# Optimization experiments

Measured on AMD Instinct MI355X. Metric: run time of the kernel, lower is better.

## Reference

```python
import jax, jax.numpy as jnp
from jax import lax
import numpy as np

DN = ('NCHW', 'OIHW', 'NCHW')


def _conv(x, w, b):
    y = lax.conv_general_dilated(x, w, (1, 1), 'SAME', dimension_numbers=DN)
    return y + b[None, :, None, None]


def setup_inputs() -> dict:
    key = jax.random.key(0)
    ks = jax.random.split(key, 8)
    B = 2
    noise = 0.1 * jax.random.normal(ks[0], (B, 768, 577), dtype=jnp.float32)  # N(0, 0.1)
    targets = jax.random.randint(ks[1], (B, 384, 384), 0, 171)
    w1 = 0.02 * jax.random.normal(ks[2], (512, 768, 3, 3), dtype=jnp.float32)
    b1 = 0.02 * jax.random.normal(ks[3], (512,), dtype=jnp.float32)
    w2 = 0.02 * jax.random.normal(ks[4], (512, 512, 3, 3), dtype=jnp.float32)
    b2 = 0.02 * jax.random.normal(ks[5], (512,), dtype=jnp.float32)
    w3 = 0.2 * jax.random.normal(ks[6], (77,), dtype=jnp.float32)  # Con3: Conv2d(1,77,1x1)
    b3 = 0.2 * jax.random.normal(ks[7], (77,), dtype=jnp.float32)
    return {'noise': noise, 'targets': targets, 'w1': w1, 'b1': b1,
            'w2': w2, 'b2': b2, 'w3': w3, 'b3': b3}


def reference(noise, targets, w1, b1, w2, b2, w3, b3):
    B = noise.shape[0]
    # NoiseToImage is shadowed by an empty nn.Sequential() -> identity
    image_noise = jnp.transpose(noise, (2, 0, 1))  # (577, B, 768)

    # --- NoiseToText ---
    H, W = targets.shape[1], targets.shape[2]
    ih = (jnp.arange(24) * H) // 24  # nearest-neighbor interpolate indices
    iw = (jnp.arange(24) * W) // 24
    m = targets[:, ih][:, :, iw]  # (B, 24, 24) class labels
    # one-hot scatter into 256 channels, keep first 171 (labels >=171 -> all-zero)
    mask = (m[:, None] == jnp.arange(171)[None, :, None, None]).astype(noise.dtype)  # (B,171,24,24)

    x = noise[:, :, 1:].reshape(B, 768, 24, 24)  # drop CLS token
    xm = x[:, None] * mask[:, :, None]            # (B,171,768,24,24)
    xm = xm.reshape(B * 171, 768, 24, 24)

    y = _conv(xm, w1, b1)                         # (B*171,512,24,24)
    y = y.reshape(-1, 512, 6, 4, 6, 4).mean(axis=(3, 5))  # AdaptiveAvgPool2d((6,6))
    y = _conv(y, w2, b2)                          # (B*171,512,6,6)
    y = y.mean(axis=(2, 3))                       # AdaptiveAvgPool2d((1,1)) -> (B*171,512)
    y = y.reshape(B, 171, 1, 512).transpose(0, 2, 1, 3)  # (B,1,171,512)
    # Con3: 1x1 conv with in_channels=1, out_channels=77
    text_noise = w3[None, :, None, None] * y + b3[None, :, None, None]  # (B,77,171,512)
    return image_noise, text_noise
```

## Files before the change

### kernel.cpp

```cpp
#include <hip/hip_runtime.h>
#include <hip/hip_bf16.h>

typedef unsigned short u16;
typedef short bf16x8 __attribute__((ext_vector_type(8)));
typedef float f32x4 __attribute__((ext_vector_type(4)));

__device__ __forceinline__ u16 f2bf(float f){
    unsigned u = __float_as_uint(f);
    unsigned r = 0x7fffu + ((u >> 16) & 1u);
    return (u16)((u + r) >> 16);
}

__device__ __forceinline__ void gload_lds16(const u16* g, u16* lds_base){
    __builtin_amdgcn_global_load_lds(
        (const __attribute__((address_space(1))) unsigned int*)g,
        (__attribute__((address_space(3))) unsigned int*)lds_base, 16, 0, 0);
}

__device__ __forceinline__ void wgbar(){
    asm volatile("" ::: "memory");
    __builtin_amdgcn_s_barrier();
    asm volatile("" ::: "memory");
}

#define OUT0_N 886272
#define OUT1_N 13483008
#define YN 175104
#define KS2 12

__global__ void k_prep(const float* __restrict__ noise, const int* __restrict__ targets,
                       const float* __restrict__ w1, const float* __restrict__ b1,
                       const float* __restrict__ w2,
                       float* __restrict__ out0, u16* __restrict__ XbfT,
                       u16* __restrict__ Are, u16* __restrict__ Mfull16,
                       float* __restrict__ biasH, int* __restrict__ labels,
                       u16* __restrict__ Zcat16){
    __shared__ float sh[32 * 33];
    int blk = blockIdx.x;
    int tid = threadIdx.x;
    if (blk < 912){
        int b   = blk / 456;
        int rem = blk % 456;
        int cb  = rem / 19, sb = rem % 19;
        int tx = tid & 31, ty = tid >> 5;
        int s0 = sb * 32, c0 = cb * 32;
        float (*tile)[33] = (float(*)[33])sh;
        #pragma unroll
        for (int i = 0; i < 4; i++){
            int c = c0 + ty + i * 8;
            int s = s0 + tx;
            if (s < 577) tile[ty + i * 8][tx] = noise[(size_t)(b * 768 + c) * 577 + s];
        }
        __syncthreads();
        #pragma unroll
        for (int i = 0; i < 4; i++){
            int s = s0 + ty + i * 8;
            int c = c0 + tx;
            if (s >= 577) continue;
            float v = tile[tx][ty + i * 8];
            out0[(size_t)(s * 2 + b) * 768 + c] = v;
            if (s >= 1) XbfT[(size_t)(b * 576 + s - 1) * 768 + c] = f2bf(v);
        }
    } else if (blk < 2448){
        int idx = (blk - 912) * 256 + tid;
        int k = idx % 768; int c1 = idx / 768;
        const float* wp = w1 + (size_t)idx * 9;
        #pragma unroll
        for (int tap = 0; tap < 9; tap++)
            Are[(size_t)(c1 * 9 + tap) * 768 + k] = f2bf(wp[tap]);
    } else if (blk < 3472){
        int b2i = blk - 2448;
        int c2 = b2i >> 1, h = b2i & 1;
        int c1 = h * 256 + tid;
        const float* wp = w2 + (size_t)(c2 * 512 + c1) * 9;
        float t[3][3];
        #pragma unroll
        for (int r = 0; r < 3; r++)
            #pragma unroll
            for (int s = 0; s < 3; s++)
                t[r][s] = wp[r * 3 + s];
        float cs0[3], cs1[3], cs2[3];
        #pragma unroll
        for (int r = 0; r < 3; r++){
            cs0[r] = t[r][0] + t[r][1];
            cs1[r] = t[r][0] + t[r][1] + t[r][2];
            cs2[r] = t[r][1] + t[r][2];
        }
        const float inv = 1.0f / 576.0f;
        u16* Mp = Mfull16 + (size_t)(c2 * 512 + c1) * 9;
        Mp[0] = f2bf(inv * (cs0[0] + cs0[1]));
        Mp[1] = f2bf(inv * (cs1[0] + cs1[1]));
        Mp[2] = f2bf(inv * (cs2[0] + cs2[1]));
        Mp[3] = f2bf(inv * (cs0[0] + cs0[1] + cs0[2]));
        Mp[4] = f2bf(inv * (cs1[0] + cs1[1] + cs1[2]));
        Mp[5] = f2bf(inv * (cs2[0] + cs2[1] + cs2[2]));
        Mp[6] = f2bf(inv * (cs0[1] + cs0[2]));
        Mp[7] = f2bf(inv * (cs1[1] + cs1[2]));
        Mp[8] = f2bf(inv * (cs2[1] + cs2[2]));
        float s_cw = 25.f * (t[0][0] + t[0][2] + t[2][0] + t[2][2])
                   + 30.f * (t[0][1] + t[1][0] + t[1][2] + t[2][1])
                   + 36.f * t[1][1];
        sh[tid] = b1[c1] * s_cw;
        __syncthreads();
        for (int o = 128; o > 0; o >>= 1){ if (tid < o) sh[tid] += sh[tid + o]; __syncthreads(); }
        if (tid == 0) biasH[h * 512 + c2] = sh[0] * (1.0f / 36.0f);
    } else if (blk < 3477){
        int idx = (blk - 3472) * 256 + tid;
        if (idx < 1152){
            int b = idx / 576; int p = idx % 576;
            int i = p / 24, j = p % 24;
            labels[idx] = targets[b * 147456 + i * 16 * 384 + j * 16];
        }
    } else {
        int idx = (blk - 3477) * 256 + tid;
        if (idx < 193536) Zcat16[342 * 4608 + idx] = 0;
    }
}

__launch_bounds__(256)
__global__ void k_gemm1(const u16* __restrict__ Are, const u16* __restrict__ XbfT,
                        float* __restrict__ D){
    __shared__ u16 As[2][192 * 64];
    __shared__ u16 Bs[2][128 * 64];
    int tid  = threadIdx.x;
    int wave = tid >> 6, lane = tid & 63;
    int l16 = lane & 15, quad = lane >> 4;
    int wm = wave >> 1, wn = wave & 1;
    int m0 = blockIdx.x * 192;
    int n0 = blockIdx.y * 128;
    int srow = lane >> 3;
    int scol = ((lane & 7) * 8) ^ (srow * 8);
    int rx   = (l16 & 7) * 8;
    const u16* Ag = Are  + (size_t)(m0 + srow) * 768 + scol;
    const u16* Bg = XbfT + (size_t)(n0 + srow) * 768 + scol;
    f32x4 acc[6][4] = {};

    auto stage = [&](int buf, int k0){
        #pragma unroll
        for (int j = 0; j < 6; j++){
            int ch = wave * 6 + j;
            gload_lds16(Ag + (size_t)ch * 8 * 768 + k0, &As[buf][ch * 512]);
        }
        #pragma unroll
        for (int j = 0; j < 4; j++){
            int ch = wave * 4 + j;
            gload_lds16(Bg + (size_t)ch * 8 * 768 + k0, &Bs[buf][ch * 512]);
        }
    };
    auto compute = [&](int buf){
        #pragma unroll
        for (int ks = 0; ks < 2; ks++){
            int kc = (ks * 32 + quad * 8) ^ rx;
            bf16x8 af[6], bf[4];
            #pragma unroll
            for (int i = 0; i < 6; i++)
                af[i] = *(const bf16x8*)&As[buf][(wm * 96 + i * 16 + l16) * 64 + kc];
            #pragma unroll
            for (int i = 0; i < 4; i++)
                bf[i] = *(const bf16x8*)&Bs[buf][(wn * 64 + i * 16 + l16) * 64 + kc];
            #pragma unroll
            for (int mi = 0; mi < 6; mi++)
                #pragma unroll
                for (int ni = 0; ni < 4; ni++)
                    acc[mi][ni] = __builtin_amdgcn_mfma_f32_16x16x32_bf16(af[mi], bf[ni], acc[mi][ni], 0, 0, 0);
        }
    };

    stage(0, 0);
    #pragma unroll 1
    for (int t = 0; t < 10; t += 2){
        stage(1, (t + 1) * 64);
        asm volatile("s_waitcnt vmcnt(10)" ::: "memory");
        wgbar();
        compute(0);
        wgbar();
        stage(0, (t + 2) * 64);
        asm volatile("s_waitcnt vmcnt(10)" ::: "memory");
        wgbar();
        compute(1);
        wgbar();
    }
    stage(1, 11 * 64);
    asm volatile("s_waitcnt vmcnt(10)" ::: "memory");
    wgbar();
    compute(0);
    wgbar();
    asm volatile("s_waitcnt vmcnt(0)" ::: "memory");
    wgbar();
    compute(1);

    #pragma unroll
    for (int mi = 0; mi < 6; mi++)
        #pragma unroll
        for (int ni = 0; ni < 4; ni++)
            #pragma unroll
            for (int r = 0; r < 4; r++)
                D[(size_t)(m0 + wm * 96 + mi * 16 + quad * 4 + r) * 1152 + n0 + wn * 64 + ni * 16 + l16] = acc[mi][ni][r];
}

__launch_bounds__(256)
__global__ void k_scatter(const float* __restrict__ D, const int* __restrict__ labels,
                          u16* __restrict__ Zcat16){
    int blk = blockIdx.x;
    int b  = blk >> 9;
    int c1 = blk & 511;
    __shared__ float acc[171 * 9];
    int t = threadIdx.x;
    for (int q = t; q < 1539; q += 256) acc[q] = 0.f;
    __syncthreads();
    for (int p = t; p < 576; p += 256){
        int cls = labels[b * 576 + p];
        if (cls < 0 || cls >= 171) continue;
        int i = p / 24, j = p % 24;
        float slot[9];
        #pragma unroll
        for (int q = 0; q < 9; q++) slot[q] = 0.f;
        unsigned used = 0;
        int tau[3]; bool vs[3];
        #pragma unroll
        for (int s1 = 0; s1 < 3; s1++){
            int v = j - s1 + 1;
            vs[s1]  = (v >= 0 && v < 24);
            tau[s1] = (v < 4) ? 0 : ((v < 20) ? 1 : 2);
        }
        #pragma unroll
        for (int r1 = 0; r1 < 3; r1++){
            int u = i - r1 + 1;
            if (u < 0 || u >= 24) continue;
            int rho = (u < 4) ? 0 : ((u < 20) ? 1 : 2);
            #pragma unroll
            for (int s1 = 0; s1 < 3; s1++){
                if (!vs[s1]) continue;
                float tv = D[(size_t)(c1 * 9 + r1 * 3 + s1) * 1152 + b * 576 + p];
                int sl = rho * 3 + tau[s1];
                slot[sl] += tv;
                used |= 1u << sl;
            }
        }
        #pragma unroll
        for (int sl = 0; sl < 9; sl++)
            if (used & (1u << sl)) atomicAdd(&acc[cls * 9 + sl], slot[sl]);
    }
    __syncthreads();
    for (int q = t; q < 1539; q += 256){
        int cls = q / 9, sl = q % 9;
        Zcat16[(size_t)(b * 171 + cls) * 4608 + c1 * 9 + sl] = f2bf(acc[q]);
    }
}

__launch_bounds__(256)
__global__ void k_gemm2m(const u16* __restrict__ Zcat16, const u16* __restrict__ Mfull16,
                         float* __restrict__ ypart){
    __shared__ u16 As[128 * 64];
    __shared__ u16 Bs[64 * 64];
    int tid  = threadIdx.x;
    int wave = tid >> 6, lane = tid & 63;
    int l16 = lane & 15, quad = lane >> 4;
    int wm = wave >> 1, wn = wave & 1;
    int m0 = blockIdx.x * 128;
    int n0 = blockIdx.y * 64;
    int kbeg = blockIdx.z * 384;
    int srow = lane >> 3, scol = (lane & 7) * 8;
    f32x4 acc[4][2] = {};
    for (int k0 = kbeg; k0 < kbeg + 384; k0 += 64){
        #pragma unroll
        for (int j = 0; j < 4; j++){
            int ch = wave * 4 + j;
            gload_lds16(Zcat16 + (size_t)(m0 + ch * 8 + srow) * 4608 + k0 + scol, &As[ch * 512]);
        }
        #pragma unroll
        for (int j = 0; j < 2; j++){
            int ch = wave * 2 + j;
            gload_lds16(Mfull16 + (size_t)(n0 + ch * 8 + srow) * 4608 + k0 + scol, &Bs[ch * 512]);
        }
        __syncthreads();
        #pragma unroll
        for (int ks = 0; ks < 2; ks++){
            bf16x8 af[4], bf[2];
            #pragma unroll
            for (int i = 0; i < 4; i++)
                af[i] = *(const bf16x8*)&As[(wm * 64 + i * 16 + l16) * 64 + ks * 32 + quad * 8];
            #pragma unroll
            for (int i = 0; i < 2; i++)
                bf[i] = *(const bf16x8*)&Bs[(wn * 32 + i * 16 + l16) * 64 + ks * 32 + quad * 8];
            #pragma unroll
            for (int mi = 0; mi < 4; mi++)
                #pragma unroll
                for (int ni = 0; ni < 2; ni++)
                    acc[mi][ni] = __builtin_amdgcn_mfma_f32_16x16x32_bf16(af[mi], bf[ni], acc[mi][ni], 0, 0, 0);
        }
        __syncthreads();
    }
    float* yp = ypart + (size_t)blockIdx.z * YN;
    #pragma unroll
    for (int mi = 0; mi < 4; mi++)
        #pragma unroll
        for (int r = 0; r < 4; r++){
            int n = m0 + wm * 64 + mi * 16 + quad * 4 + r;
            if (n >= 342) continue;
            #pragma unroll
            for (int ni = 0; ni < 2; ni++)
                yp[(size_t)n * 512 + n0 + wn * 32 + ni * 16 + l16] = acc[mi][ni][r];
        }
}

__global__ void k_red(const float* __restrict__ ypart, const float* __restrict__ biasH,
                      const float* __restrict__ b2, float4* __restrict__ ysum){
    int idx = blockIdx.x * 128 + threadIdx.x;
    int c4 = idx & 127;
    int n  = idx >> 7;
    float4 sum = ((const float4*)b2)[c4];
    float4 ba  = ((const float4*)biasH)[c4];
    float4 bb  = ((const float4*)biasH)[128 + c4];
    sum.x += ba.x + bb.x; sum.y += ba.y + bb.y; sum.z += ba.z + bb.z; sum.w += ba.w + bb.w;
    #pragma unroll
    for (int s = 0; s < KS2; s++){
        float4 v = *(const float4*)&ypart[(size_t)s * YN + (size_t)n * 512 + c4 * 4];
        sum.x += v.x; sum.y += v.y; sum.z += v.z; sum.w += v.w;
    }
    ysum[idx] = sum;
}

__global__ void k_expand(const float4* __restrict__ ysum, const float* __restrict__ w3,
                         const float* __restrict__ b3, float4* __restrict__ out1){
    int idx = blockIdx.x * 256 + threadIdx.x;
    if (idx >= OUT1_N / 4) return;
    int c4 = idx & 127;
    int t  = idx >> 7;
    int cls = t % 171;
    int u   = t / 171;
    int o   = u % 77;
    int b   = u / 77;
    float w  = w3[o];
    float bb = b3[o];
    float4 v = ysum[(b * 171 + cls) * 128 + c4];
    out1[idx] = make_float4(w * v.x + bb, w * v.y + bb, w * v.z + bb, w * v.w + bb);
}

extern "C" void kernel_launch(void* const* d_in, const int* in_sizes, int n_in,
                              void* d_out, int out_size, void* d_ws, size_t ws_size,
                              hipStream_t stream) {
    const float* noise   = (const float*)d_in[0];
    const int*   targets = (const int*)  d_in[1];
    const float* w1      = (const float*)d_in[2];
    const float* b1      = (const float*)d_in[3];
    const float* w2      = (const float*)d_in[4];
    const float* b2      = (const float*)d_in[5];
    const float* w3      = (const float*)d_in[6];
    const float* b3      = (const float*)d_in[7];
    float* out0 = (float*)d_out;
    float* out1 = out0 + OUT0_N;

    char* ws = (char*)d_ws;
    const size_t OFF_ARE  = 0;
    const size_t OFF_X    = 7077888;
    const size_t OFF_D    = OFF_X   + 1769472;
    const size_t OFF_MF   = OFF_D   + 21233664;
    const size_t OFF_ZC   = OFF_MF  + 4718592;
    const size_t OFF_BH   = OFF_ZC  + 3538944;
    const size_t OFF_LAB  = OFF_BH  + 4096;
    const size_t OFF_YS   = OFF_LAB + 4608;

    u16*   Are    = (u16*)  (ws + OFF_ARE);
    u16*   XbfT   = (u16*)  (ws + OFF_X);
    float* D      = (float*)(ws + OFF_D);
    float* ypart  = (float*)(ws + OFF_D);
    u16*   Mfull16= (u16*)  (ws + OFF_MF);
    u16*   Zcat16 = (u16*)  (ws + OFF_ZC);
    float* biasH  = (float*)(ws + OFF_BH);
    int*   labels = (int*)  (ws + OFF_LAB);
    float* ysum   = (float*)(ws + OFF_YS);

    k_prep  <<<4233, 256, 0, stream>>>(noise, targets, w1, b1, w2,
                                       out0, XbfT, Are, Mfull16, biasH, labels, Zcat16);
    k_gemm1 <<<dim3(24, 9), 256, 0, stream>>>(Are, XbfT, D);
    k_scatter<<<1024, 256, 0, stream>>>(D, labels, Zcat16);
    k_gemm2m<<<dim3(3, 8, KS2), 256, 0, stream>>>(Zcat16, Mfull16, ypart);
    k_red   <<<342, 128, 0, stream>>>(ypart, biasH, b2, (float4*)ysum);
    k_expand<<<13167, 256, 0, stream>>>((const float4*)ysum, w3, b3, (float4*)out1);
}
```

Baseline: 156.2 us.

## Store GEMM1 output as bf16, atomically reduce split-K GEMM2, drop reduction kernel

GEMM1 now writes its intermediate as bf16 instead of fp32, which halves the traffic for that write and for the scatter kernel's reads. GEMM2's split-K partials are atomically added into a zero-initialised ysum (zeroed by extra k_prep blocks), and the bias additions move into k_expand. This removes the separate k_red kernel and its partial buffer. s_setprio is also placed around the MFMA loops. Rounding D to bf16 adds precision loss, and fp32 atomics make the summation order nondeterministic.

```diff
diff --git a/kernel.cpp b/kernel.cpp
--- a/kernel.cpp
+++ b/kernel.cpp
@@ -9,6 +9,9 @@
     unsigned u = __float_as_uint(f);
     unsigned r = 0x7fffu + ((u >> 16) & 1u);
     return (u16)((u + r) >> 16);
+}
+__device__ __forceinline__ float bf2f(u16 h){
+    return __uint_as_float(((unsigned)h) << 16);
 }
 
 __device__ __forceinline__ void gload_lds16(const u16* g, u16* lds_base){
@@ -34,7 +37,7 @@
                        float* __restrict__ out0, u16* __restrict__ XbfT,
                        u16* __restrict__ Are, u16* __restrict__ Mfull16,
                        float* __restrict__ biasH, int* __restrict__ labels,
-                       u16* __restrict__ Zcat16){
+                       u16* __restrict__ Zcat16, float4* __restrict__ ysum){
     __shared__ float sh[32 * 33];
     int blk = blockIdx.x;
     int tid = threadIdx.x;
@@ -111,15 +114,18 @@
             int i = p / 24, j = p % 24;
             labels[idx] = targets[b * 147456 + i * 16 * 384 + j * 16];
         }
-    } else {
+    } else if (blk < 4233){
         int idx = (blk - 3477) * 256 + tid;
         if (idx < 193536) Zcat16[342 * 4608 + idx] = 0;
+    } else {
+        int idx = (blk - 4233) * 256 + tid;
+        ysum[idx] = make_float4(0.f, 0.f, 0.f, 0.f);
     }
 }
 
 __launch_bounds__(256)
 __global__ void k_gemm1(const u16* __restrict__ Are, const u16* __restrict__ XbfT,
-                        float* __restrict__ D){
+                        u16* __restrict__ D){
     __shared__ u16 As[2][192 * 64];
     __shared__ u16 Bs[2][128 * 64];
     int tid  = threadIdx.x;
@@ -158,11 +164,13 @@
             #pragma unroll
             for (int i = 0; i < 4; i++)
                 bf[i] = *(const bf16x8*)&Bs[buf][(wn * 64 + i * 16 + l16) * 64 + kc];
+            __builtin_amdgcn_s_setprio(1);
             #pragma unroll
             for (int mi = 0; mi < 6; mi++)
                 #pragma unroll
                 for (int ni = 0; ni < 4; ni++)
                     acc[mi][ni] = __builtin_amdgcn_mfma_f32_16x16x32_bf16(af[mi], bf[ni], acc[mi][ni], 0, 0, 0);
+            __builtin_amdgcn_s_setprio(0);
         }
     };
 
@@ -195,11 +203,11 @@
         for (int ni = 0; ni < 4; ni++)
             #pragma unroll
             for (int r = 0; r < 4; r++)
-                D[(size_t)(m0 + wm * 96 + mi * 16 + quad * 4 + r) * 1152 + n0 + wn * 64 + ni * 16 + l16] = acc[mi][ni][r];
+                D[(size_t)(m0 + wm * 96 + mi * 16 + quad * 4 + r) * 1152 + n0 + wn * 64 + ni * 16 + l16] = f2bf(acc[mi][ni][r]);
 }
 
 __launch_bounds__(256)
-__global__ void k_scatter(const float* __restrict__ D, const int* __restrict__ labels,
+__global__ void k_scatter(const u16* __restrict__ D, const int* __restrict__ labels,
                           u16* __restrict__ Zcat16){
     int blk = blockIdx.x;
     int b  = blk >> 9;
@@ -231,7 +239,7 @@
             #pragma unroll
             for (int s1 = 0; s1 < 3; s1++){
                 if (!vs[s1]) continue;
-                float tv = D[(size_t)(c1 * 9 + r1 * 3 + s1) * 1152 + b * 576 + p];
+                float tv = bf2f(D[(size_t)(c1 * 9 + r1 * 3 + s1) * 1152 + b * 576 + p]);
                 int sl = rho * 3 + tau[s1];
                 slot[sl] += tv;
                 used |= 1u << sl;
@@ -250,7 +258,7 @@
 
 __launch_bounds__(256)
 __global__ void k_gemm2m(const u16* __restrict__ Zcat16, const u16* __restrict__ Mfull16,
-                         float* __restrict__ ypart){
+                         float* __restrict__ ysum){
     __shared__ u16 As[128 * 64];
     __shared__ u16 Bs[64 * 64];
     int tid  = threadIdx.x;
@@ -283,15 +291,16 @@
             #pragma unroll
             for (int i = 0; i < 2; i++)
                 bf[i] = *(const bf16x8*)&Bs[(wn * 32 + i * 16 + l16) * 64 + ks * 32 + quad * 8];
+            __builtin_amdgcn_s_setprio(1);
             #pragma unroll
             for (int mi = 0; mi < 4; mi++)
                 #pragma unroll
                 for (int ni = 0; ni < 2; ni++)
                     acc[mi][ni] = __builtin_amdgcn_mfma_f32_16x16x32_bf16(af[mi], bf[ni], acc[mi][ni], 0, 0, 0);
+            __builtin_amdgcn_s_setprio(0);
         }
         __syncthreads();
     }
-    float* yp = ypart + (size_t)blockIdx.z * YN;
     #pragma unroll
     for (int mi = 0; mi < 4; mi++)
         #pragma unroll
@@ -300,28 +309,12 @@
             if (n >= 342) continue;
             #pragma unroll
             for (int ni = 0; ni < 2; ni++)
-                yp[(size_t)n * 512 + n0 + wn * 32 + ni * 16 + l16] = acc[mi][ni][r];
-        }
-}
-
-__global__ void k_red(const float* __restrict__ ypart, const float* __restrict__ biasH,
-                      const float* __restrict__ b2, float4* __restrict__ ysum){
-    int idx = blockIdx.x * 128 + threadIdx.x;
-    int c4 = idx & 127;
-    int n  = idx >> 7;
-    float4 sum = ((const float4*)b2)[c4];
-    float4 ba  = ((const float4*)biasH)[c4];
-    float4 bb  = ((const float4*)biasH)[128 + c4];
-    sum.x += ba.x + bb.x; sum.y += ba.y + bb.y; sum.z += ba.z + bb.z; sum.w += ba.w + bb.w;
-    #pragma unroll
-    for (int s = 0; s < KS2; s++){
-        float4 v = *(const float4*)&ypart[(size_t)s * YN + (size_t)n * 512 + c4 * 4];
-        sum.x += v.x; sum.y += v.y; sum.z += v.z; sum.w += v.w;
-    }
-    ysum[idx] = sum;
-}
-
-__global__ void k_expand(const float4* __restrict__ ysum, const float* __restrict__ w3,
+                atomicAdd(&ysum[(size_t)n * 512 + n0 + wn * 32 + ni * 16 + l16], acc[mi][ni][r]);
+        }
+}
+
+__global__ void k_expand(const float4* __restrict__ ysum, const float* __restrict__ biasH,
+                         const float* __restrict__ b2, const float* __restrict__ w3,
                          const float* __restrict__ b3, float4* __restrict__ out1){
     int idx = blockIdx.x * 256 + threadIdx.x;
     if (idx >= OUT1_N / 4) return;
@@ -333,7 +326,14 @@
     int b   = u / 77;
     float w  = w3[o];
     float bb = b3[o];
-    float4 v = ysum[(b * 171 + cls) * 128 + c4];
+    float4 v  = ysum[(b * 171 + cls) * 128 + c4];
+    float4 s2 = ((const float4*)b2)[c4];
+    float4 ba = ((const float4*)biasH)[c4];
+    float4 bc = ((const float4*)biasH)[128 + c4];
+    v.x += s2.x + ba.x + bc.x;
+    v.y += s2.y + ba.y + bc.y;
+    v.z += s2.z + ba.z + bc.z;
+    v.w += s2.w + ba.w + bc.w;
     out1[idx] = make_float4(w * v.x + bb, w * v.y + bb, w * v.z + bb, w * v.w + bb);
 }
 
@@ -355,7 +355,7 @@
     const size_t OFF_ARE  = 0;
     const size_t OFF_X    = 7077888;
     const size_t OFF_D    = OFF_X   + 1769472;
-    const size_t OFF_MF   = OFF_D   + 21233664;
+    const size_t OFF_MF   = OFF_D   + 10616832;
     const size_t OFF_ZC   = OFF_MF  + 4718592;
     const size_t OFF_BH   = OFF_ZC  + 3538944;
     const size_t OFF_LAB  = OFF_BH  + 4096;
@@ -363,19 +363,18 @@
 
     u16*   Are    = (u16*)  (ws + OFF_ARE);
     u16*   XbfT   = (u16*)  (ws + OFF_X);
-    float* D      = (float*)(ws + OFF_D);
-    float* ypart  = (float*)(ws + OFF_D);
+    u16*   D      = (u16*)  (ws + OFF_D);
     u16*   Mfull16= (u16*)  (ws + OFF_MF);
     u16*   Zcat16 = (u16*)  (ws + OFF_ZC);
     float* biasH  = (float*)(ws + OFF_BH);
     int*   labels = (int*)  (ws + OFF_LAB);
     float* ysum   = (float*)(ws + OFF_YS);
 
-    k_prep  <<<4233, 256, 0, stream>>>(noise, targets, w1, b1, w2,
-                                       out0, XbfT, Are, Mfull16, biasH, labels, Zcat16);
+    k_prep  <<<4404, 256, 0, stream>>>(noise, targets, w1, b1, w2,
+                                       out0, XbfT, Are, Mfull16, biasH, labels, Zcat16,
+                                       (float4*)ysum);
     k_gemm1 <<<dim3(24, 9), 256, 0, stream>>>(Are, XbfT, D);
     k_scatter<<<1024, 256, 0, stream>>>(D, labels, Zcat16);
-    k_gemm2m<<<dim3(3, 8, KS2), 256, 0, stream>>>(Zcat16, Mfull16, ypart);
-    k_red   <<<342, 128, 0, stream>>>(ypart, biasH, b2, (float4*)ysum);
-    k_expand<<<13167, 256, 0, stream>>>((const float4*)ysum, w3, b3, (float4*)out1);
-}
+    k_gemm2m<<<dim3(3, 8, KS2), 256, 0, stream>>>(Zcat16, Mfull16, ysum);
+    k_expand<<<13167, 256, 0, stream>>>((const float4*)ysum, biasH, b2, w3, b3, (float4*)out1);
+}
```

Result: slower. 160.5 us (+2.8%).
